# Performance work log

Hardware: AMD Instinct MI355X
Metric: run time of the kernel (lower is better)

Reference implementation:

```python
import jax, jax.numpy as jnp
import numpy as np

G = 8          # grid_size
N = G * G      # 64 nodes
DEG = 17       # neighbors per node for 8x8 sudoku (2x4 boxes)
STEPS = 32
H = 96         # hidden_dim
E = 16         # embed_size
B = 16         # batch


def sudoku_edges():
    # row (7) + col (7) + 2x4 box (7) neighbors, set-union -> 17 per node
    idx = np.arange(N).reshape(G, G)
    nb = []
    for j in range(N):
        r, c = j // G, j % G
        br, bc = (r // 2) * 2, (c // 4) * 4
        s = set(idx[r, :].tolist()) | set(idx[:, c].tolist()) | set(idx[br:br + 2, bc:bc + 4].flatten().tolist())
        s.discard(j)
        nb.append(sorted(s))
    return np.asarray(nb, dtype=np.int32)  # [64, 17]


def setup_inputs() -> dict:
    key = jax.random.key(0)
    ks = jax.random.split(key, 16)
    sc = 0.05
    inp = {
        "x": jax.random.randint(ks[0], (B, G, G), 0, G + 1),            # given digits, 0 = blank
        "target": jax.random.randint(ks[1], (B, G, G), 0, G) + 1,       # solutions in 1..8
        "edges": jnp.asarray(sudoku_edges()),                            # [64, 17] int32
        "digit_emb": jax.random.normal(ks[2], (G + 1, E), jnp.float32) * sc,
        "row_emb": jax.random.normal(ks[3], (G, E), jnp.float32) * sc,
        "col_emb": jax.random.normal(ks[4], (G, E), jnp.float32) * sc,
        "in0_W": jax.random.normal(ks[5], (3 * E, H), jnp.float32) * sc,
        "in0_b": jnp.zeros((H,), jnp.float32),
        "in_Ws": jax.random.normal(ks[6], (3, H, H), jnp.float32) * sc,
        "in_bs": jnp.zeros((3, H), jnp.float32),
        "msg0_W": jax.random.normal(ks[7], (2 * H, H), jnp.float32) * sc,
        "msg0_b": jnp.zeros((H,), jnp.float32),
        "msg_Ws": jax.random.normal(ks[8], (3, H, H), jnp.float32) * sc,
        "msg_bs": jnp.zeros((3, H), jnp.float32),
        "W_ih": jax.random.normal(ks[9], (2 * H, 4 * H), jnp.float32) * sc,
        "W_hh": jax.random.normal(ks[10], (H, 4 * H), jnp.float32) * sc,
        "b_ih": jnp.zeros((4 * H,), jnp.float32),
        "b_hh": jnp.zeros((4 * H,), jnp.float32),
        "pred_W": jax.random.normal(ks[11], (H, G), jnp.float32) * sc,
        "pred_b": jnp.zeros((G,), jnp.float32),
    }
    return inp


def _mlp(z, W0, b0, Ws, bs):
    # Linear -> ReLU -> Linear -> ReLU -> Linear -> ReLU -> Linear (def_MLP)
    z = jax.nn.relu(z @ W0 + b0)
    z = jax.nn.relu(z @ Ws[0] + bs[0])
    z = jax.nn.relu(z @ Ws[1] + bs[1])
    return z @ Ws[2] + bs[2]


def reference(x, target, edges, digit_emb, row_emb, col_emb,
              in0_W, in0_b, in_Ws, in_bs,
              msg0_W, msg0_b, msg_Ws, msg_bs,
              W_ih, W_hh, b_ih, b_hh, pred_W, pred_b):
    bsz = x.shape[0]
    xf = x.reshape(bsz, N)
    tgt = target.reshape(bsz, N) - 1                      # labels 0..7

    de = digit_emb[xf]                                    # [B,64,E]
    re = row_emb[jnp.repeat(jnp.arange(G), G)]            # [64,E]
    ce = col_emb[jnp.tile(jnp.arange(G), G)]              # [64,E]
    feat = jnp.concatenate([de,
                            jnp.broadcast_to(re[None], (bsz, N, E)),
                            jnp.broadcast_to(ce[None], (bsz, N, E))], axis=-1)
    xin = _mlp(feat, in0_W, in0_b, in_Ws, in_bs)          # [B,64,H]

    h0 = jnp.zeros((bsz, N, H), jnp.float32)
    s0 = jnp.zeros((bsz * N, H), jnp.float32)

    def step(carry, _):
        h, s, loss = carry
        # gather-by-edge message passing
        h_edges = h[:, edges]                                             # [B,64,17,H]
        h_self = jnp.broadcast_to(h[:, :, None, :], (bsz, N, DEG, H))
        msg = _mlp(jnp.concatenate([h_edges, h_self], -1),
                   msg0_W, msg0_b, msg_Ws, msg_bs).sum(axis=2)            # [B,64,H]
        # LSTMCell update
        lstm_in = jnp.concatenate([msg, xin], -1).reshape(bsz * N, 2 * H)
        gates = lstm_in @ W_ih + b_ih + h.reshape(bsz * N, H) @ W_hh + b_hh
        i, f, g, o = jnp.split(gates, 4, axis=-1)
        s2 = jax.nn.sigmoid(f) * s + jax.nn.sigmoid(i) * jnp.tanh(g)
        h2 = (jax.nn.sigmoid(o) * jnp.tanh(s2)).reshape(bsz, N, H)
        # per-step prediction / loss / accuracy
        logp = jax.nn.log_softmax(h2 @ pred_W + pred_b, axis=-1)          # [B,64,8]
        pred = jnp.argmax(logp, axis=-1)
        acc = jnp.mean(jnp.all(pred == tgt, axis=1).astype(jnp.float32))
        loss_n = -jnp.sum(jnp.take_along_axis(logp, tgt[..., None], -1)) / (bsz * N)
        return (h2, s2, loss + loss_n), acc

    (h, s, loss), accs = jax.lax.scan(step, (h0, s0, jnp.float32(0.0)), None, length=STEPS)
    loss = loss / STEPS
    final_pred = jnp.argmax(h @ pred_W + pred_b, axis=-1)                 # [B,64]
    return loss, accs, final_pred
```

## Files before the change

kernel.cpp:

```cpp
#include <hip/hip_runtime.h>

#define DEG 17
#define NSTEPS 32
#define HD 96

#define WS_U0     0
#define WS_BAR    196608
#define WS_U1     196864
#define WS_XIN    393472
#define WS_GX     491776
#define WS_LOSSP  884992
#define WS_CNTP   901376

#define W1L   0
#define W2L   9216
#define MSGB  18432
#define M0B   18720
#define VBASE 18816
#define VSTR  10272
#define VZ1    0
#define VZ2    3840
#define VGX    7680
#define VGATES 8448
#define VMSGH  9216
#define VS3T   9600
#define VH2T   9792
#define VSLC   9984
#define VLGT   10176
#define VNBRI  10208
#define BARC  (VBASE + 2*VSTR)
#define SMTOT (BARC + 8)

__global__ void init_kernel(
    const int* __restrict__ x,
    const float* __restrict__ digit_emb,
    const float* __restrict__ row_emb,
    const float* __restrict__ col_emb,
    const float* __restrict__ in0_W,
    const float* __restrict__ in0_b,
    const float* __restrict__ in_Ws,
    const float* __restrict__ in_bs,
    const float* __restrict__ msg0_b,
    float* __restrict__ xin,
    float* __restrict__ u0)
{
  const int node = blockIdx.x;
  const int j = threadIdx.x;
  const int n = node & 63;
  const int r = n >> 3, c = n & 7;
  __shared__ float feat[48];
  __shared__ float za[HD];
  __shared__ float zb[HD];
  if (j < 16)      feat[j] = digit_emb[x[node]*16 + j];
  else if (j < 32) feat[j] = row_emb[r*16 + (j-16)];
  else if (j < 48) feat[j] = col_emb[c*16 + (j-32)];
  u0[node*192 + 96 + j] = msg0_b[j];
  __syncthreads();
  float a = in0_b[j];
  for (int k = 0; k < 48; ++k) a = fmaf(feat[k], in0_W[k*HD + j], a);
  za[j] = fmaxf(a, 0.f);
  __syncthreads();
  a = in_bs[j];
  for (int k = 0; k < HD; ++k) a = fmaf(za[k], in_Ws[k*HD + j], a);
  zb[j] = fmaxf(a, 0.f);
  __syncthreads();
  a = in_bs[HD + j];
  for (int k = 0; k < HD; ++k) a = fmaf(zb[k], in_Ws[9216 + k*HD + j], a);
  za[j] = fmaxf(a, 0.f);
  __syncthreads();
  a = in_bs[2*HD + j];
  for (int k = 0; k < HD; ++k) a = fmaf(za[k], in_Ws[2*9216 + k*HD + j], a);
  xin[node*HD + j] = a;
}

__global__ __launch_bounds__(384) void gx_kernel(
    const float* __restrict__ xin, const float* __restrict__ W_ih,
    const float* __restrict__ b_ih, const float* __restrict__ b_hh,
    float* __restrict__ gx)
{
  __shared__ float xs[4*HD];
  const int tid = threadIdx.x;
  const int base = blockIdx.x * 4;
  {
    const int m = tid / HD, k = tid - m*HD;
    xs[m*HD + k] = xin[(base+m)*HD + k];
  }
  __syncthreads();
  const int j = tid;
  float a0 = b_ih[j] + b_hh[j], a1 = a0, a2 = a0, a3 = a0;
  for (int k = 0; k < HD; ++k) {
    const float w = W_ih[(96+k)*384 + j];
    a0 = fmaf(xs[k], w, a0);
    a1 = fmaf(xs[HD+k], w, a1);
    a2 = fmaf(xs[2*HD+k], w, a2);
    a3 = fmaf(xs[3*HD+k], w, a3);
  }
  gx[(base+0)*384 + j] = a0;
  gx[(base+1)*384 + j] = a1;
  gx[(base+2)*384 + j] = a2;
  gx[(base+3)*384 + j] = a3;
}

__device__ __forceinline__ void vbar(int* c, int want) {
  if ((threadIdx.x & 63) == 0)
    __hip_atomic_fetch_add(c, 1, __ATOMIC_RELEASE, __HIP_MEMORY_SCOPE_WORKGROUP);
  while (__hip_atomic_load(c, __ATOMIC_ACQUIRE, __HIP_MEMORY_SCOPE_WORKGROUP) < want)
    __builtin_amdgcn_s_sleep(1);
}

__global__ __launch_bounds__(512, 1) void solve_kernel(
    const int* __restrict__ edges,
    const float* __restrict__ msg0_W, const float* __restrict__ msg0_b,
    const float* __restrict__ msg_Ws, const float* __restrict__ msg_bs,
    const float* __restrict__ W_ih, const float* __restrict__ W_hh,
    const float* __restrict__ pred_W, const float* __restrict__ pred_b,
    const int* __restrict__ target,
    const float* __restrict__ gx,
    float* __restrict__ u0, float* __restrict__ u1,
    int* bar,
    float* __restrict__ lossP, int* __restrict__ cntP,
    float* __restrict__ final_pred_out)
{
  __shared__ float sm[SMTOT];

  const int tid = threadIdx.x;
  const int vb  = tid >> 8;
  const int vt  = tid & 255;
  const int blk = blockIdx.x;
  const int bb  = blk & 15;
  const int grp = blk >> 4;
  const int base = bb*64 + grp*4;
  const int gbase = base + vb*2;

  float* const vs = sm + VBASE + vb*VSTR;
  int* const vnbri = (int*)(vs + VNBRI);
  int* const vbc = (int*)(sm + BARC) + vb;

  for (int i = tid*4; i < 9216; i += 2048) {
    *(float4*)&sm[W1L + i] = *(const float4*)&msg_Ws[i];
    *(float4*)&sm[W2L + i] = *(const float4*)&msg_Ws[9216 + i];
  }
  if (tid < 288) sm[MSGB + tid] = msg_bs[tid];
  if (tid < 96)  sm[M0B + tid]  = msg0_b[tid];
  if (tid < 2)   ((int*)(sm + BARC))[tid] = 0;
  #pragma unroll
  for (int t = 0; t < 3; ++t) {
    const int idx = t*256 + vt;
    vs[VGX + idx] = gx[gbase*384 + idx];
  }
  if (vt < 192) {
    vs[VSLC + vt] = 0.f;
    vs[VMSGH + 192 + vt] = 0.f;
  }
  if (vt < 40) {
    const int m = vt / 20, r = vt % 20;
    vnbri[vt] = (r < DEG) ? (bb*64 + edges[((grp*4 + vb*2) + m)*DEG + r])*192 : -1;
  }
  __syncthreads();

  const float* uP = u0;
  float*       uN = u1;
  int vph = 0;

  for (int st = 0; st < NSTEPS; ++st) {
    if (vt < 240) {
      const int row = vt % 40;
      const int kh  = vt / 40;
      const int m = row / 20;
      const int k0 = kh * 16;
      const int nb = vnbri[row];
      if (nb >= 0) {
        const float* ue = uP + nb + k0;
        const float* us = uP + (gbase+m)*192 + 96 + k0;
        #pragma unroll
        for (int t = 0; t < 4; ++t) {
          const float4 a = *(const float4*)(ue + 4*t);
          const float4 b = *(const float4*)(us + 4*t);
          vs[VZ1 + (k0+4*t+0)*40 + row] = fmaxf(a.x + b.x, 0.f);
          vs[VZ1 + (k0+4*t+1)*40 + row] = fmaxf(a.y + b.y, 0.f);
          vs[VZ1 + (k0+4*t+2)*40 + row] = fmaxf(a.z + b.z, 0.f);
          vs[VZ1 + (k0+4*t+3)*40 + row] = fmaxf(a.w + b.w, 0.f);
        }
      } else {
        #pragma unroll
        for (int t = 0; t < 16; ++t) vs[VZ1 + (k0+t)*40 + row] = 0.f;
      }
    } else {
      const int i = vt - 240;
      #pragma unroll
      for (int t = 0; t < 12; ++t) vs[VS3T + i*12 + t] = 0.f;
    }
    vph += 4; vbar(vbc, vph);

    if (vt < 240) {
      const int jg = vt % 24, dg = vt / 24;
      const int j4 = jg*4, d4 = dg*4;
      float acc[4][4] = {{0.f}};
      #pragma unroll 4
      for (int k = 0; k < 96; ++k) {
        const float4 z = *(const float4*)&vs[VZ1 + k*40 + d4];
        const float4 w = *(const float4*)&sm[W1L + k*96 + j4];
        const float ze[4] = {z.x, z.y, z.z, z.w};
        const float we[4] = {w.x, w.y, w.z, w.w};
        #pragma unroll
        for (int dd = 0; dd < 4; ++dd)
          #pragma unroll
          for (int jj = 0; jj < 4; ++jj)
            acc[dd][jj] = fmaf(ze[dd], we[jj], acc[dd][jj]);
      }
      #pragma unroll
      for (int jj = 0; jj < 4; ++jj) {
        const float b1 = sm[MSGB + j4 + jj];
        float4 q;
        q.x = fmaxf(acc[0][jj] + b1, 0.f);
        q.y = fmaxf(acc[1][jj] + b1, 0.f);
        q.z = fmaxf(acc[2][jj] + b1, 0.f);
        q.w = fmaxf(acc[3][jj] + b1, 0.f);
        *(float4*)&vs[VZ2 + (j4+jj)*40 + d4] = q;
      }
    }
    vph += 4; vbar(vbc, vph);

    if (vt < 240) {
      const int jg = vt % 24, dg = vt / 24;
      const int j4 = jg*4, d4 = dg*4;
      float acc[4][4] = {{0.f}};
      #pragma unroll 4
      for (int k = 0; k < 96; ++k) {
        const float4 z = *(const float4*)&vs[VZ2 + k*40 + d4];
        const float4 w = *(const float4*)&sm[W2L + k*96 + j4];
        const float ze[4] = {z.x, z.y, z.z, z.w};
        const float we[4] = {w.x, w.y, w.z, w.w};
        #pragma unroll
        for (int dd = 0; dd < 4; ++dd)
          #pragma unroll
          for (int jj = 0; jj < 4; ++jj)
            acc[dd][jj] = fmaf(ze[dd], we[jj], acc[dd][jj]);
      }
      const int nd = d4 / 20;
      const int r0 = d4 - nd*20;
      #pragma unroll
      for (int jj = 0; jj < 4; ++jj) {
        const float b2 = sm[MSGB + 96 + j4 + jj];
        float p = 0.f;
        #pragma unroll
        for (int dd = 0; dd < 4; ++dd)
          if (r0 + dd < DEG) p += fmaxf(acc[dd][jj] + b2, 0.f);
        atomicAdd(&vs[VS3T + (j4+jj)*2 + nd], p);
      }
    }
    vph += 4; vbar(vbc, vph);

    if (vt < 192) {
      const int jg = vt % 24, kq = vt / 24;
      const int j4 = jg*4, k0 = kq*12;
      const float* W3 = msg_Ws + 2*9216;
      float acc[2][4] = {{0.f}};
      #pragma unroll
      for (int kk = 0; kk < 12; ++kk) {
        const int k = k0 + kk;
        const float2 sv = *(const float2*)&vs[VS3T + k*2];
        const float4 wv = *(const float4*)&W3[k*96 + j4];
        const float se[2] = {sv.x, sv.y};
        const float we[4] = {wv.x, wv.y, wv.z, wv.w};
        #pragma unroll
        for (int m = 0; m < 2; ++m)
          #pragma unroll
          for (int jj = 0; jj < 4; ++jj)
            acc[m][jj] = fmaf(se[m], we[jj], acc[m][jj]);
      }
      #pragma unroll
      for (int m = 0; m < 2; ++m) {
        float4 q = {acc[m][0], acc[m][1], acc[m][2], acc[m][3]};
        *(float4*)&vs[VZ1 + (kq*2 + m)*96 + j4] = q;
      }
    }
    vph += 4; vbar(vbc, vph);
    if (vt < 192) {
      const int m = vt / 96, j = vt % 96;
      float v = 17.f * sm[MSGB + 192 + j];
      #pragma unroll
      for (int kq = 0; kq < 8; ++kq) v += vs[VZ1 + (kq*2 + m)*96 + j];
      vs[VMSGH + j*2 + m] = v;
    }
    vph += 4; vbar(vbc, vph);

    {
      const int jg = vt & 63, kq = vt >> 6;
      const int j6 = jg*6, k0 = kq*48;
      const float* Wb = (k0 < 96) ? (W_ih + (size_t)k0*384) : (W_hh + (size_t)(k0-96)*384);
      float acc[2][6] = {{0.f}};
      #pragma unroll 4
      for (int kk = 0; kk < 48; ++kk) {
        const float2 iv = *(const float2*)&vs[VMSGH + (k0+kk)*2];
        const float* wp = Wb + kk*384 + j6;
        const float2 wa = *(const float2*)wp;
        const float2 wb2 = *(const float2*)(wp + 2);
        const float2 wc = *(const float2*)(wp + 4);
        const float ie[2] = {iv.x, iv.y};
        const float we[6] = {wa.x, wa.y, wb2.x, wb2.y, wc.x, wc.y};
        #pragma unroll
        for (int m = 0; m < 2; ++m)
          #pragma unroll
          for (int jj = 0; jj < 6; ++jj)
            acc[m][jj] = fmaf(ie[m], we[jj], acc[m][jj]);
      }
      #pragma unroll
      for (int m = 0; m < 2; ++m) {
        float2 qa = {acc[m][0], acc[m][1]};
        float2 qb = {acc[m][2], acc[m][3]};
        float2 qc = {acc[m][4], acc[m][5]};
        *(float2*)&vs[VZ1 + (kq*2 + m)*384 + j6]     = qa;
        *(float2*)&vs[VZ1 + (kq*2 + m)*384 + j6 + 2] = qb;
        *(float2*)&vs[VZ1 + (kq*2 + m)*384 + j6 + 4] = qc;
      }
    }
    vph += 4; vbar(vbc, vph);
    {
      #pragma unroll
      for (int t = 0; t < 3; ++t) {
        const int idx = t*256 + vt;
        const int m = idx / 384, j = idx - m*384;
        float gv = vs[VGX + idx];
        #pragma unroll
        for (int kq = 0; kq < 4; ++kq) gv += vs[VZ1 + (kq*2 + m)*384 + j];
        vs[VGATES + idx] = gv;
      }
    }
    vph += 4; vbar(vbc, vph);

    if (vt < 192) {
      const int m = vt / 96, hj = vt - m*96;
      const float gi = vs[VGATES + m*384 + hj];
      const float gf = vs[VGATES + m*384 + 96 + hj];
      const float gg = vs[VGATES + m*384 + 192 + hj];
      const float go = vs[VGATES + m*384 + 288 + hj];
      const float sv = vs[VSLC + vt];
      const float ig = 1.f/(1.f + expf(-gi));
      const float fg = 1.f/(1.f + expf(-gf));
      const float cg = tanhf(gg);
      const float og = 1.f/(1.f + expf(-go));
      const float s2 = fg*sv + ig*cg;
      const float h2 = og*tanhf(s2);
      vs[VSLC + vt] = s2;
      vs[VH2T + hj*2 + m] = h2;
      vs[VMSGH + (96+hj)*2 + m] = h2;
    }
    vph += 4; vbar(vbc, vph);

    {
      const int jg = vt & 31, kq = vt >> 5;
      const int j6 = jg*6, k0 = kq*12;
      const float* Wb = (j6 < 96) ? (msg0_W + j6) : (msg0_W + 9216 + j6 - 96);
      float acc[2][6] = {{0.f}};
      #pragma unroll
      for (int kk = 0; kk < 12; ++kk) {
        const int k = k0 + kk;
        const float2 iv = *(const float2*)&vs[VH2T + k*2];
        const float* wp = Wb + k*96;
        const float2 wa = *(const float2*)wp;
        const float2 wb2 = *(const float2*)(wp + 2);
        const float2 wc = *(const float2*)(wp + 4);
        const float ie[2] = {iv.x, iv.y};
        const float we[6] = {wa.x, wa.y, wb2.x, wb2.y, wc.x, wc.y};
        #pragma unroll
        for (int m = 0; m < 2; ++m)
          #pragma unroll
          for (int jj = 0; jj < 6; ++jj)
            acc[m][jj] = fmaf(ie[m], we[jj], acc[m][jj]);
      }
      #pragma unroll
      for (int m = 0; m < 2; ++m) {
        float2 qa = {acc[m][0], acc[m][1]};
        float2 qb = {acc[m][2], acc[m][3]};
        float2 qc = {acc[m][4], acc[m][5]};
        *(float2*)&vs[VZ1 + (kq*2 + m)*192 + j6]     = qa;
        *(float2*)&vs[VZ1 + (kq*2 + m)*192 + j6 + 2] = qb;
        *(float2*)&vs[VZ1 + (kq*2 + m)*192 + j6 + 4] = qc;
      }
    }
    vph += 4; vbar(vbc, vph);
    if (vt < 192) {
      #pragma unroll
      for (int t = 0; t < 2; ++t) {
        const int idx = t*192 + vt;
        const int m = idx / 192, j = idx - m*192;
        float v = (j >= 96) ? sm[M0B + j - 96] : 0.f;
        #pragma unroll
        for (int kq = 0; kq < 8; ++kq) v += vs[VZ1 + (kq*2 + m)*192 + j];
        uN[(gbase+m)*192 + j] = v;
      }
    } else {
      const int t2 = vt - 192;
      const int m = t2 >> 5, c = (t2 >> 2) & 7, kq2 = t2 & 3;
      float p = 0.f;
      #pragma unroll
      for (int kk = 0; kk < 24; ++kk) {
        const int k = kq2*24 + kk;
        p = fmaf(vs[VH2T + k*2 + m], pred_W[k*8 + c], p);
      }
      p += __shfl_xor(p, 1);
      p += __shfl_xor(p, 2);
      if (kq2 == 0) vs[VLGT + m*8 + c] = p + pred_b[c];
    }
    vph += 4; vbar(vbc, vph);

    if (vt < 2) {
      const int m = vt;
      const int node = gbase + m;
      float mx = vs[VLGT + m*8];
      int pred = 0;
      #pragma unroll
      for (int c = 1; c < 8; ++c) {
        const float v = vs[VLGT + m*8 + c];
        if (v > mx) { mx = v; pred = c; }
      }
      float sum = 0.f;
      #pragma unroll
      for (int c = 0; c < 8; ++c) sum += expf(vs[VLGT + m*8 + c] - mx);
      const float lse = mx + logf(sum);
      const int tgt = target[node] - 1;
      vs[VLGT + 16 + m] = lse - vs[VLGT + m*8 + tgt];
      vs[VLGT + 20 + m] = (pred == tgt) ? 1.f : 0.f;
      if (st == NSTEPS-1) final_pred_out[node] = (float)pred;
      if (m == 0) {
        lossP[st*512 + bb*32 + grp*2 + vb] = vs[VLGT+16] + vs[VLGT+17];
        cntP[st*512 + bb*32 + grp*2 + vb] = (int)(vs[VLGT+20] + vs[VLGT+21]);
      }
    }

    if (st < NSTEPS-1) {
      __syncthreads();
      if (tid == 0) {
        __hip_atomic_fetch_add(&bar[bb*16], 1, __ATOMIC_RELEASE, __HIP_MEMORY_SCOPE_AGENT);
        const int want = 16*(st+1);
        while (__hip_atomic_load(&bar[bb*16], __ATOMIC_RELAXED, __HIP_MEMORY_SCOPE_AGENT) < want)
          __builtin_amdgcn_s_sleep(2);
        __threadfence();
      }
      __syncthreads();
      float* tp = (float*)uP; uP = uN; uN = tp;
    }
  }
}

__global__ void finalize_kernel(const float* __restrict__ lossP,
                                const int* __restrict__ cntP,
                                float* __restrict__ out)
{
  __shared__ float sl[32];
  const int tid = threadIdx.x;
  const int st = tid >> 3, q = tid & 7;
  float lsum = 0.f;
  for (int i = 0; i < 64; ++i) lsum += lossP[st*512 + q*64 + i];
  lsum += __shfl_xor(lsum, 1);
  lsum += __shfl_xor(lsum, 2);
  lsum += __shfl_xor(lsum, 4);
  if (q == 0) sl[st] = lsum;
  float okc = 0.f;
  #pragma unroll
  for (int t = 0; t < 2; ++t) {
    const int bbat = q + 8*t;
    int c = 0;
    for (int i = 0; i < 32; ++i) c += cntP[st*512 + bbat*32 + i];
    okc += (c == 64) ? 1.f : 0.f;
  }
  okc += __shfl_xor(okc, 1);
  okc += __shfl_xor(okc, 2);
  okc += __shfl_xor(okc, 4);
  if (q == 0) out[1 + st] = okc / 16.f;
  __syncthreads();
  if (tid == 0) {
    float tot = 0.f;
    for (int i = 0; i < 32; ++i) tot += sl[i];
    out[0] = tot / (1024.f * (float)NSTEPS);
  }
}

extern "C" void kernel_launch(void* const* d_in, const int* in_sizes, int n_in,
                              void* d_out, int out_size, void* d_ws, size_t ws_size,
                              hipStream_t stream) {
  const int*   x         = (const int*)  d_in[0];
  const int*   target    = (const int*)  d_in[1];
  const int*   edges     = (const int*)  d_in[2];
  const float* digit_emb = (const float*)d_in[3];
  const float* row_emb   = (const float*)d_in[4];
  const float* col_emb   = (const float*)d_in[5];
  const float* in0_W     = (const float*)d_in[6];
  const float* in0_b     = (const float*)d_in[7];
  const float* in_Ws     = (const float*)d_in[8];
  const float* in_bs     = (const float*)d_in[9];
  const float* msg0_W    = (const float*)d_in[10];
  const float* msg0_b    = (const float*)d_in[11];
  const float* msg_Ws    = (const float*)d_in[12];
  const float* msg_bs    = (const float*)d_in[13];
  const float* W_ih      = (const float*)d_in[14];
  const float* W_hh      = (const float*)d_in[15];
  const float* b_ih      = (const float*)d_in[16];
  const float* b_hh      = (const float*)d_in[17];
  const float* pred_W    = (const float*)d_in[18];
  const float* pred_b    = (const float*)d_in[19];

  float* ws    = (float*)d_ws;
  float* u0    = ws + WS_U0;
  int*   bar   = (int*)(ws + WS_BAR);
  float* u1    = ws + WS_U1;
  float* xin   = ws + WS_XIN;
  float* gxb   = ws + WS_GX;
  float* lossP = ws + WS_LOSSP;
  int*   cntP  = (int*)(ws + WS_CNTP);

  hipMemsetAsync(d_ws, 0, (size_t)(196608 + 256)*sizeof(float), stream);

  init_kernel<<<1024, HD, 0, stream>>>(x, digit_emb, row_emb, col_emb,
                                       in0_W, in0_b, in_Ws, in_bs,
                                       msg0_b, xin, u0);
  gx_kernel<<<256, 384, 0, stream>>>(xin, W_ih, b_ih, b_hh, gxb);

  float* outp = (float*)d_out;
  solve_kernel<<<256, 512, 0, stream>>>(
      edges, msg0_W, msg0_b, msg_Ws, msg_bs,
      W_ih, W_hh, pred_W, pred_b, target, gxb,
      u0, u1, bar, lossP, cntP, outp + 1 + NSTEPS);

  finalize_kernel<<<1, 256, 0, stream>>>(lossP, cntP, outp);
}
```

Baseline: 1.034 ms.

## Use packed FMA, split-K LSTM gate matmul, per-half-block grid barrier

The accumulation loops switch to packed two-wide float FMAs (v_pk_fma_f32) in the message MLP and gate matmuls. The W3 output now goes straight into the message vector through shared atomics, which removes one reduction phase and one barrier. The gate and msg0 matmuls are re-tiled with more K-splits and 12-wide column tiles. pred_W is staged in shared memory, and the block-wide __syncthreads around the cross-block barrier is replaced by per-half-block arrival, doubling the counter target. Risks include extra reduction passes over more partial sums, float atomics changing summation order, and subtle memory ordering in the new barrier scheme.

```diff
diff --git a/kernel.cpp b/kernel.cpp
--- a/kernel.cpp
+++ b/kernel.cpp
@@ -3,6 +3,16 @@
 #define DEG 17
 #define NSTEPS 32
 #define HD 96
+
+typedef float v2f __attribute__((ext_vector_type(2)));
+
+#if __has_builtin(__builtin_elementwise_fma)
+#define PFMA(a,b,c) __builtin_elementwise_fma(a,b,c)
+#else
+static __device__ __forceinline__ v2f PFMA(v2f a, v2f b, v2f c) {
+  v2f r; r[0] = fmaf(a[0], b[0], c[0]); r[1] = fmaf(a[1], b[1], c[1]); return r;
+}
+#endif
 
 #define WS_U0     0
 #define WS_BAR    196608
@@ -16,7 +26,8 @@
 #define W2L   9216
 #define MSGB  18432
 #define M0B   18720
-#define VBASE 18816
+#define PRW   18816
+#define VBASE 19584
 #define VSTR  10272
 #define VZ1    0
 #define VZ2    3840
@@ -129,8 +140,7 @@
   const int blk = blockIdx.x;
   const int bb  = blk & 15;
   const int grp = blk >> 4;
-  const int base = bb*64 + grp*4;
-  const int gbase = base + vb*2;
+  const int gbase = bb*64 + grp*4 + vb*2;
 
   float* const vs = sm + VBASE + vb*VSTR;
   int* const vnbri = (int*)(vs + VNBRI);
@@ -143,6 +153,7 @@
   if (tid < 288) sm[MSGB + tid] = msg_bs[tid];
   if (tid < 96)  sm[M0B + tid]  = msg0_b[tid];
   if (tid < 2)   ((int*)(sm + BARC))[tid] = 0;
+  for (int i = tid; i < 768; i += 512) sm[PRW + i] = pred_W[i];
   #pragma unroll
   for (int t = 0; t < 3; ++t) {
     const int idx = t*256 + vt;
@@ -189,33 +200,39 @@
       const int i = vt - 240;
       #pragma unroll
       for (int t = 0; t < 12; ++t) vs[VS3T + i*12 + t] = 0.f;
+      #pragma unroll
+      for (int t = 0; t < 12; ++t) {
+        const int idx = i*12 + t;
+        vs[VMSGH + idx] = 17.f * sm[MSGB + 192 + (idx >> 1)];
+      }
     }
     vph += 4; vbar(vbc, vph);
 
     if (vt < 240) {
       const int jg = vt % 24, dg = vt / 24;
       const int j4 = jg*4, d4 = dg*4;
-      float acc[4][4] = {{0.f}};
+      v2f acc[4][2] = {};
       #pragma unroll 4
       for (int k = 0; k < 96; ++k) {
         const float4 z = *(const float4*)&vs[VZ1 + k*40 + d4];
         const float4 w = *(const float4*)&sm[W1L + k*96 + j4];
+        const v2f w01 = {w.x, w.y}, w23 = {w.z, w.w};
         const float ze[4] = {z.x, z.y, z.z, z.w};
-        const float we[4] = {w.x, w.y, w.z, w.w};
-        #pragma unroll
-        for (int dd = 0; dd < 4; ++dd)
-          #pragma unroll
-          for (int jj = 0; jj < 4; ++jj)
-            acc[dd][jj] = fmaf(ze[dd], we[jj], acc[dd][jj]);
+        #pragma unroll
+        for (int dd = 0; dd < 4; ++dd) {
+          const v2f zz = {ze[dd], ze[dd]};
+          acc[dd][0] = PFMA(zz, w01, acc[dd][0]);
+          acc[dd][1] = PFMA(zz, w23, acc[dd][1]);
+        }
       }
       #pragma unroll
       for (int jj = 0; jj < 4; ++jj) {
         const float b1 = sm[MSGB + j4 + jj];
         float4 q;
-        q.x = fmaxf(acc[0][jj] + b1, 0.f);
-        q.y = fmaxf(acc[1][jj] + b1, 0.f);
-        q.z = fmaxf(acc[2][jj] + b1, 0.f);
-        q.w = fmaxf(acc[3][jj] + b1, 0.f);
+        q.x = fmaxf(acc[0][jj>>1][jj&1] + b1, 0.f);
+        q.y = fmaxf(acc[1][jj>>1][jj&1] + b1, 0.f);
+        q.z = fmaxf(acc[2][jj>>1][jj&1] + b1, 0.f);
+        q.w = fmaxf(acc[3][jj>>1][jj&1] + b1, 0.f);
         *(float4*)&vs[VZ2 + (j4+jj)*40 + d4] = q;
       }
     }
@@ -224,18 +241,19 @@
     if (vt < 240) {
       const int jg = vt % 24, dg = vt / 24;
       const int j4 = jg*4, d4 = dg*4;
-      float acc[4][4] = {{0.f}};
+      v2f acc[4][2] = {};
       #pragma unroll 4
       for (int k = 0; k < 96; ++k) {
         const float4 z = *(const float4*)&vs[VZ2 + k*40 + d4];
         const float4 w = *(const float4*)&sm[W2L + k*96 + j4];
+        const v2f w01 = {w.x, w.y}, w23 = {w.z, w.w};
         const float ze[4] = {z.x, z.y, z.z, z.w};
-        const float we[4] = {w.x, w.y, w.z, w.w};
-        #pragma unroll
-        for (int dd = 0; dd < 4; ++dd)
-          #pragma unroll
-          for (int jj = 0; jj < 4; ++jj)
-            acc[dd][jj] = fmaf(ze[dd], we[jj], acc[dd][jj]);
+        #pragma unroll
+        for (int dd = 0; dd < 4; ++dd) {
+          const v2f zz = {ze[dd], ze[dd]};
+          acc[dd][0] = PFMA(zz, w01, acc[dd][0]);
+          acc[dd][1] = PFMA(zz, w23, acc[dd][1]);
+        }
       }
       const int nd = d4 / 20;
       const int r0 = d4 - nd*20;
@@ -245,7 +263,7 @@
         float p = 0.f;
         #pragma unroll
         for (int dd = 0; dd < 4; ++dd)
-          if (r0 + dd < DEG) p += fmaxf(acc[dd][jj] + b2, 0.f);
+          if (r0 + dd < DEG) p += fmaxf(acc[dd][jj>>1][jj&1] + b2, 0.f);
         atomicAdd(&vs[VS3T + (j4+jj)*2 + nd], p);
       }
     }
@@ -255,64 +273,65 @@
       const int jg = vt % 24, kq = vt / 24;
       const int j4 = jg*4, k0 = kq*12;
       const float* W3 = msg_Ws + 2*9216;
-      float acc[2][4] = {{0.f}};
+      v2f acc[2][2] = {};
       #pragma unroll
       for (int kk = 0; kk < 12; ++kk) {
         const int k = k0 + kk;
         const float2 sv = *(const float2*)&vs[VS3T + k*2];
         const float4 wv = *(const float4*)&W3[k*96 + j4];
-        const float se[2] = {sv.x, sv.y};
-        const float we[4] = {wv.x, wv.y, wv.z, wv.w};
-        #pragma unroll
-        for (int m = 0; m < 2; ++m)
-          #pragma unroll
-          for (int jj = 0; jj < 4; ++jj)
-            acc[m][jj] = fmaf(se[m], we[jj], acc[m][jj]);
+        const v2f w01 = {wv.x, wv.y}, w23 = {wv.z, wv.w};
+        const v2f s0 = {sv.x, sv.x}, s1 = {sv.y, sv.y};
+        acc[0][0] = PFMA(s0, w01, acc[0][0]);
+        acc[0][1] = PFMA(s0, w23, acc[0][1]);
+        acc[1][0] = PFMA(s1, w01, acc[1][0]);
+        acc[1][1] = PFMA(s1, w23, acc[1][1]);
+      }
+      #pragma unroll
+      for (int m = 0; m < 2; ++m)
+        #pragma unroll
+        for (int jj = 0; jj < 4; ++jj)
+          atomicAdd(&vs[VMSGH + (j4+jj)*2 + m], acc[m][jj>>1][jj&1]);
+    }
+    vph += 4; vbar(vbc, vph);
+
+    {
+      const int jg = vt & 31, kq = vt >> 5;
+      const int j12 = jg*12, k0 = kq*24;
+      const float* Wb = (kq < 4) ? (W_ih + (size_t)k0*384 + j12)
+                                 : (W_hh + (size_t)(k0-96)*384 + j12);
+      v2f acc[2][6] = {};
+      #pragma unroll 4
+      for (int kk = 0; kk < 24; ++kk) {
+        const float2 iv = *(const float2*)&vs[VMSGH + (k0+kk)*2];
+        const float* wp = Wb + kk*384;
+        const float4 wa = *(const float4*)wp;
+        const float4 wm = *(const float4*)(wp + 4);
+        const float4 wc = *(const float4*)(wp + 8);
+        const v2f w0 = {wa.x, wa.y}, w1 = {wa.z, wa.w};
+        const v2f w2 = {wm.x, wm.y}, w3 = {wm.z, wm.w};
+        const v2f w4 = {wc.x, wc.y}, w5 = {wc.z, wc.w};
+        const v2f i0 = {iv.x, iv.x}, i1 = {iv.y, iv.y};
+        acc[0][0] = PFMA(i0, w0, acc[0][0]);
+        acc[0][1] = PFMA(i0, w1, acc[0][1]);
+        acc[0][2] = PFMA(i0, w2, acc[0][2]);
+        acc[0][3] = PFMA(i0, w3, acc[0][3]);
+        acc[0][4] = PFMA(i0, w4, acc[0][4]);
+        acc[0][5] = PFMA(i0, w5, acc[0][5]);
+        acc[1][0] = PFMA(i1, w0, acc[1][0]);
+        acc[1][1] = PFMA(i1, w1, acc[1][1]);
+        acc[1][2] = PFMA(i1, w2, acc[1][2]);
+        acc[1][3] = PFMA(i1, w3, acc[1][3]);
+        acc[1][4] = PFMA(i1, w4, acc[1][4]);
+        acc[1][5] = PFMA(i1, w5, acc[1][5]);
       }
       #pragma unroll
       for (int m = 0; m < 2; ++m) {
-        float4 q = {acc[m][0], acc[m][1], acc[m][2], acc[m][3]};
-        *(float4*)&vs[VZ1 + (kq*2 + m)*96 + j4] = q;
-      }
-    }
-    vph += 4; vbar(vbc, vph);
-    if (vt < 192) {
-      const int m = vt / 96, j = vt % 96;
-      float v = 17.f * sm[MSGB + 192 + j];
-      #pragma unroll
-      for (int kq = 0; kq < 8; ++kq) v += vs[VZ1 + (kq*2 + m)*96 + j];
-      vs[VMSGH + j*2 + m] = v;
-    }
-    vph += 4; vbar(vbc, vph);
-
-    {
-      const int jg = vt & 63, kq = vt >> 6;
-      const int j6 = jg*6, k0 = kq*48;
-      const float* Wb = (k0 < 96) ? (W_ih + (size_t)k0*384) : (W_hh + (size_t)(k0-96)*384);
-      float acc[2][6] = {{0.f}};
-      #pragma unroll 4
-      for (int kk = 0; kk < 48; ++kk) {
-        const float2 iv = *(const float2*)&vs[VMSGH + (k0+kk)*2];
-        const float* wp = Wb + kk*384 + j6;
-        const float2 wa = *(const float2*)wp;
-        const float2 wb2 = *(const float2*)(wp + 2);
-        const float2 wc = *(const float2*)(wp + 4);
-        const float ie[2] = {iv.x, iv.y};
-        const float we[6] = {wa.x, wa.y, wb2.x, wb2.y, wc.x, wc.y};
-        #pragma unroll
-        for (int m = 0; m < 2; ++m)
-          #pragma unroll
-          for (int jj = 0; jj < 6; ++jj)
-            acc[m][jj] = fmaf(ie[m], we[jj], acc[m][jj]);
-      }
-      #pragma unroll
-      for (int m = 0; m < 2; ++m) {
-        float2 qa = {acc[m][0], acc[m][1]};
-        float2 qb = {acc[m][2], acc[m][3]};
-        float2 qc = {acc[m][4], acc[m][5]};
-        *(float2*)&vs[VZ1 + (kq*2 + m)*384 + j6]     = qa;
-        *(float2*)&vs[VZ1 + (kq*2 + m)*384 + j6 + 2] = qb;
-        *(float2*)&vs[VZ1 + (kq*2 + m)*384 + j6 + 4] = qc;
+        float4 qa = {acc[m][0][0], acc[m][0][1], acc[m][1][0], acc[m][1][1]};
+        float4 qb = {acc[m][2][0], acc[m][2][1], acc[m][3][0], acc[m][3][1]};
+        float4 qc = {acc[m][4][0], acc[m][4][1], acc[m][5][0], acc[m][5][1]};
+        *(float4*)&vs[VZ1 + (kq*2 + m)*384 + j12]     = qa;
+        *(float4*)&vs[VZ1 + (kq*2 + m)*384 + j12 + 4] = qb;
+        *(float4*)&vs[VZ1 + (kq*2 + m)*384 + j12 + 8] = qc;
       }
     }
     vph += 4; vbar(vbc, vph);
@@ -323,7 +342,7 @@
         const int m = idx / 384, j = idx - m*384;
         float gv = vs[VGX + idx];
         #pragma unroll
-        for (int kq = 0; kq < 4; ++kq) gv += vs[VZ1 + (kq*2 + m)*384 + j];
+        for (int kq = 0; kq < 8; ++kq) gv += vs[VZ1 + (kq*2 + m)*384 + j];
         vs[VGATES + idx] = gv;
       }
     }
@@ -349,34 +368,43 @@
     vph += 4; vbar(vbc, vph);
 
     {
-      const int jg = vt & 31, kq = vt >> 5;
-      const int j6 = jg*6, k0 = kq*12;
-      const float* Wb = (j6 < 96) ? (msg0_W + j6) : (msg0_W + 9216 + j6 - 96);
-      float acc[2][6] = {{0.f}};
-      #pragma unroll
-      for (int kk = 0; kk < 12; ++kk) {
+      const int jg = vt & 15, kq = vt >> 4;
+      const int j12 = jg*12, k0 = kq*6;
+      const float* Wb = (j12 < 96) ? (msg0_W + j12) : (msg0_W + 9216 + j12 - 96);
+      v2f acc[2][6] = {};
+      #pragma unroll
+      for (int kk = 0; kk < 6; ++kk) {
         const int k = k0 + kk;
         const float2 iv = *(const float2*)&vs[VH2T + k*2];
         const float* wp = Wb + k*96;
-        const float2 wa = *(const float2*)wp;
-        const float2 wb2 = *(const float2*)(wp + 2);
-        const float2 wc = *(const float2*)(wp + 4);
-        const float ie[2] = {iv.x, iv.y};
-        const float we[6] = {wa.x, wa.y, wb2.x, wb2.y, wc.x, wc.y};
-        #pragma unroll
-        for (int m = 0; m < 2; ++m)
-          #pragma unroll
-          for (int jj = 0; jj < 6; ++jj)
-            acc[m][jj] = fmaf(ie[m], we[jj], acc[m][jj]);
+        const float4 wa = *(const float4*)wp;
+        const float4 wm = *(const float4*)(wp + 4);
+        const float4 wc = *(const float4*)(wp + 8);
+        const v2f w0 = {wa.x, wa.y}, w1 = {wa.z, wa.w};
+        const v2f w2 = {wm.x, wm.y}, w3 = {wm.z, wm.w};
+        const v2f w4 = {wc.x, wc.y}, w5 = {wc.z, wc.w};
+        const v2f i0 = {iv.x, iv.x}, i1 = {iv.y, iv.y};
+        acc[0][0] = PFMA(i0, w0, acc[0][0]);
+        acc[0][1] = PFMA(i0, w1, acc[0][1]);
+        acc[0][2] = PFMA(i0, w2, acc[0][2]);
+        acc[0][3] = PFMA(i0, w3, acc[0][3]);
+        acc[0][4] = PFMA(i0, w4, acc[0][4]);
+        acc[0][5] = PFMA(i0, w5, acc[0][5]);
+        acc[1][0] = PFMA(i1, w0, acc[1][0]);
+        acc[1][1] = PFMA(i1, w1, acc[1][1]);
+        acc[1][2] = PFMA(i1, w2, acc[1][2]);
+        acc[1][3] = PFMA(i1, w3, acc[1][3]);
+        acc[1][4] = PFMA(i1, w4, acc[1][4]);
+        acc[1][5] = PFMA(i1, w5, acc[1][5]);
       }
       #pragma unroll
       for (int m = 0; m < 2; ++m) {
-        float2 qa = {acc[m][0], acc[m][1]};
-        float2 qb = {acc[m][2], acc[m][3]};
-        float2 qc = {acc[m][4], acc[m][5]};
-        *(float2*)&vs[VZ1 + (kq*2 + m)*192 + j6]     = qa;
-        *(float2*)&vs[VZ1 + (kq*2 + m)*192 + j6 + 2] = qb;
-        *(float2*)&vs[VZ1 + (kq*2 + m)*192 + j6 + 4] = qc;
+        float4 qa = {acc[m][0][0], acc[m][0][1], acc[m][1][0], acc[m][1][1]};
+        float4 qb = {acc[m][2][0], acc[m][2][1], acc[m][3][0], acc[m][3][1]};
+        float4 qc = {acc[m][4][0], acc[m][4][1], acc[m][5][0], acc[m][5][1]};
+        *(float4*)&vs[VZ1 + (kq*2 + m)*192 + j12]     = qa;
+        *(float4*)&vs[VZ1 + (kq*2 + m)*192 + j12 + 4] = qb;
+        *(float4*)&vs[VZ1 + (kq*2 + m)*192 + j12 + 8] = qc;
       }
     }
     vph += 4; vbar(vbc, vph);
@@ -387,7 +415,7 @@
         const int m = idx / 192, j = idx - m*192;
         float v = (j >= 96) ? sm[M0B + j - 96] : 0.f;
         #pragma unroll
-        for (int kq = 0; kq < 8; ++kq) v += vs[VZ1 + (kq*2 + m)*192 + j];
+        for (int kq = 0; kq < 16; ++kq) v += vs[VZ1 + (kq*2 + m)*192 + j];
         uN[(gbase+m)*192 + j] = v;
       }
     } else {
@@ -397,12 +425,13 @@
       #pragma unroll
       for (int kk = 0; kk < 24; ++kk) {
         const int k = kq2*24 + kk;
-        p = fmaf(vs[VH2T + k*2 + m], pred_W[k*8 + c], p);
+        p = fmaf(vs[VH2T + k*2 + m], sm[PRW + k*8 + c], p);
       }
       p += __shfl_xor(p, 1);
       p += __shfl_xor(p, 2);
       if (kq2 == 0) vs[VLGT + m*8 + c] = p + pred_b[c];
     }
+    __threadfence();
     vph += 4; vbar(vbc, vph);
 
     if (vt < 2) {
@@ -430,16 +459,15 @@
     }
 
     if (st < NSTEPS-1) {
-      __syncthreads();
-      if (tid == 0) {
+      if (vt == 0) {
         __hip_atomic_fetch_add(&bar[bb*16], 1, __ATOMIC_RELEASE, __HIP_MEMORY_SCOPE_AGENT);
-        const int want = 16*(st+1);
+        const int want = 32*(st+1);
         while (__hip_atomic_load(&bar[bb*16], __ATOMIC_RELAXED, __HIP_MEMORY_SCOPE_AGENT) < want)
           __builtin_amdgcn_s_sleep(2);
         __threadfence();
       }
-      __syncthreads();
-      float* tp = (float*)uP; uP = uN; uN = tp;
+      vph += 4; vbar(vbc, vph);
+      const float* tp = uP; uP = uN; uN = (float*)tp;
     }
   }
 }
```

Measured after the change: 2.159 ms. 109% more time.
